# Performance work log

Measured on AMD Instinct MI355X. Metric: run time of the kernel, lower is better.

Reference implementation:

```python
import jax, jax.numpy as jnp
import numpy as np

C = 512
NH = 8
HD = C // NH
GROUPS = 8
EPS = 1e-5

def group_norm(x, w, b):
    # x: [B,C,H,W], 8 groups
    B, Cc, H, W = x.shape
    xg = x.reshape(B, GROUPS, Cc // GROUPS, H, W)
    mu = xg.mean(axis=(2, 3, 4), keepdims=True)
    var = xg.var(axis=(2, 3, 4), keepdims=True)
    xn = (xg - mu) * jax.lax.rsqrt(var + EPS)
    xn = xn.reshape(B, Cc, H, W)
    return xn * w[None, :, None, None] + b[None, :, None, None]

def conv1x1(x, w, b):
    # w: [O,C], b: [O]
    return jnp.einsum('oc,bchw->bohw', w, x) + b[None, :, None, None]

def setup_inputs() -> dict:
    key = jax.random.key(0)
    ks = jax.random.split(key, 12)
    s = 1.0 / np.sqrt(C)
    inp = {
        'x': jax.random.normal(ks[0], (8, C, 32, 32), dtype=jnp.float32),
        'norm_w': jnp.ones((C,), jnp.float32),
        'norm_b': jnp.zeros((C,), jnp.float32),
        'qw': jax.random.uniform(ks[1], (C, C), jnp.float32, -s, s),
        'qb': jax.random.uniform(ks[2], (C,), jnp.float32, -s, s),
        'kw': jax.random.uniform(ks[3], (C, C), jnp.float32, -s, s),
        'kb': jax.random.uniform(ks[4], (C,), jnp.float32, -s, s),
        'vw': jax.random.uniform(ks[5], (C, C), jnp.float32, -s, s),
        'vb': jax.random.uniform(ks[6], (C,), jnp.float32, -s, s),
        'pw': jax.random.uniform(ks[7], (C, C), jnp.float32, -s, s),
        'pb': jax.random.uniform(ks[8], (C,), jnp.float32, -s, s),
    }
    return inp

def reference(x, norm_w, norm_b, qw, qb, kw, kb, vw, vb, pw, pb):
    b, c, h, w = x.shape
    scale = HD ** (-0.5)
    xn = group_norm(x, norm_w, norm_b)
    q = conv1x1(xn, qw, qb).reshape(b, NH, HD, h * w)
    k = conv1x1(xn, kw, kb).reshape(b, NH, HD, h * w)
    v = conv1x1(xn, vw, vb).reshape(b, NH, HD, h * w)
    attn = jnp.einsum('bhcn,bhcm->bhnm', q, k) * scale
    attn = jax.nn.softmax(attn, axis=-1)
    out = jnp.einsum('bhnm,bhcm->bhcn', attn, v)
    out = out.reshape(b, c, h, w)
    out = conv1x1(out, pw, pb)
    return out + x
```

## Files before the change

kernel.cpp:

```cpp
#include <hip/hip_runtime.h>

#define C_DIM 512
#define N_PIX 1024
#define B_DIM 8
#define NHEAD 8
#define HDIM 64
#define NGRP 8
#define CG 64
#define EPSF 1e-5f

typedef __bf16 bf16x8_t __attribute__((ext_vector_type(8)));
typedef __bf16 bf16x4_t __attribute__((ext_vector_type(4)));
typedef float  f32x4_t  __attribute__((ext_vector_type(4)));
typedef unsigned int u32x4_t __attribute__((ext_vector_type(4)));

__device__ __forceinline__ __bf16 f2b(float f) {
  unsigned int u = __builtin_bit_cast(unsigned int, f);
  u += 0x7fffu + ((u >> 16) & 1u);
  unsigned short s = (unsigned short)(u >> 16);
  return __builtin_bit_cast(__bf16, s);
}

__device__ __forceinline__ unsigned int pack_trunc(float a, float b) {
  return (__builtin_bit_cast(unsigned int, a) >> 16) |
         (__builtin_bit_cast(unsigned int, b) & 0xffff0000u);
}

__device__ __forceinline__ void async16(const void* g, void* l) {
  __builtin_amdgcn_global_load_lds((const __attribute__((address_space(1))) void*)g,
                                   (__attribute__((address_space(3))) void*)l, 16, 0, 0);
}

__global__ __launch_bounds__(256) void prep_kernel(
    const float* __restrict__ qw, const float* __restrict__ kw,
    const float* __restrict__ vw, const float* __restrict__ pw,
    __bf16* __restrict__ wb,
    const float* __restrict__ x, float2* __restrict__ psum)
{
  if (blockIdx.x < 1024) {
    int idx = blockIdx.x * 256 + threadIdx.x;
    int mat = idx >> 16;
    int off = (idx & 65535) * 4;
    const float* src = (mat == 0) ? qw : (mat == 1) ? kw : (mat == 2) ? vw : pw;
    float4 v = *(const float4*)(src + off);
    bf16x4_t pk;
    pk[0] = f2b(v.x); pk[1] = f2b(v.y); pk[2] = f2b(v.z); pk[3] = f2b(v.w);
    *(bf16x4_t*)(wb + mat * (512 * 512) + off) = pk;
  } else {
    const int t = blockIdx.x - 1024;
    const int s = t & 7, bg = t >> 3;
    const float* xp = x + ((size_t)bg * CG + s * 8) * N_PIX;
    float sum = 0.f, sum2 = 0.f;
#pragma unroll
    for (int it = 0; it < 8; it++) {
      float4 v = ((const float4*)xp)[it * 256 + threadIdx.x];
      sum  += v.x + v.y + v.z + v.w;
      sum2 += v.x * v.x + v.y * v.y + v.z * v.z + v.w * v.w;
    }
#pragma unroll
    for (int off = 32; off; off >>= 1) {
      sum  += __shfl_xor(sum, off, 64);
      sum2 += __shfl_xor(sum2, off, 64);
    }
    __shared__ float red[8];
    const int lane = threadIdx.x & 63, wv = threadIdx.x >> 6;
    if (lane == 0) { red[wv] = sum; red[4 + wv] = sum2; }
    __syncthreads();
    if (threadIdx.x == 0) {
      float s1 = red[0] + red[1] + red[2] + red[3];
      float s2 = red[4] + red[5] + red[6] + red[7];
      psum[bg * 8 + s] = make_float2(s1, s2);
    }
  }
}

__global__ __launch_bounds__(256) void gn_apply_kernel(
    const float* __restrict__ x, const float2* __restrict__ psum,
    const float* __restrict__ gw, const float* __restrict__ gb,
    __bf16* __restrict__ xnT)
{
  const int n0 = blockIdx.x * 32, b = blockIdx.y, z = blockIdx.z;
  const int tid = threadIdx.x;
  __shared__ float mu_s[8], rs_s[8];
  __shared__ __align__(16) __bf16 tile[32 * 264];

  if (tid < 8) {
    float s1 = 0.f, s2 = 0.f;
#pragma unroll
    for (int i = 0; i < 8; i++) {
      float2 p = psum[(b * 8 + tid) * 8 + i];
      s1 += p.x; s2 += p.y;
    }
    const float inv = 1.f / (float)(CG * N_PIX);
    float mu = s1 * inv;
    float var = s2 * inv - mu * mu;
    mu_s[tid] = mu;
    rs_s[tid] = rsqrtf(var + EPSF);
  }
  __syncthreads();

  const float* xb = x + (size_t)b * C_DIM * N_PIX + n0;
  const int cl = tid >> 3;
  const int nq = (tid & 7) * 4;
#pragma unroll
  for (int co = 0; co < 8; co++) {
    const int cc = co * 32 + cl;
    const int c = z * 256 + cc;
    float4 v = *(const float4*)(xb + (size_t)c * N_PIX + nq);
    const int g = c >> 6;
    const float rs = rs_s[g];
    const float a = rs * gw[c];
    const float bb = gb[c] - mu_s[g] * a;
    tile[(nq + 0) * 264 + cc] = f2b(v.x * a + bb);
    tile[(nq + 1) * 264 + cc] = f2b(v.y * a + bb);
    tile[(nq + 2) * 264 + cc] = f2b(v.z * a + bb);
    tile[(nq + 3) * 264 + cc] = f2b(v.w * a + bb);
  }
  __syncthreads();

  __bf16* dst = xnT + ((size_t)b * N_PIX + n0) * C_DIM + z * 256;
  const int l32 = tid & 31, nr = tid >> 5;
#pragma unroll
  for (int no = 0; no < 4; no++) {
    const int n = no * 8 + nr;
    const int cc = l32 * 8;
    *(bf16x8_t*)(dst + (size_t)n * C_DIM + cc) =
        *(const bf16x8_t*)(tile + n * 264 + cc);
  }
}

__device__ __forceinline__ void gemm_core_64(
    const __bf16* __restrict__ A, const __bf16* __restrict__ B,
    __bf16* As, __bf16* Bs, f32x4_t acc[2][4])
{
  const int tid  = threadIdx.x;
  const int lane = tid & 63;
  const int wv   = tid >> 6;
  const int quad = lane >> 4;
  const int l16  = lane & 15;
  const int wm = (wv >> 1) * 32;
  const int wn = (wv & 1) * 64;
  const int swq = (quad ^ ((l16 >> 1) & 3)) * 8;

  f32x4_t zero = {0.f, 0.f, 0.f, 0.f};
#pragma unroll
  for (int i = 0; i < 2; i++)
#pragma unroll
    for (int j = 0; j < 4; j++) acc[i][j] = zero;

  const int chA  = wv * 64 + lane;
  const int rA = chA >> 2;
  const int kA = ((chA & 3) ^ ((rA >> 1) & 3)) * 8;
  const int chB0 = wv * 64 + lane, chB1 = 256 + wv * 64 + lane;
  const int rB0 = chB0 >> 2, kB0 = ((chB0 & 3) ^ ((rB0 >> 1) & 3)) * 8;
  const int rB1 = chB1 >> 2, kB1 = ((chB1 & 3) ^ ((rB1 >> 1) & 3)) * 8;

  async16(A + (size_t)rA * 512 + kA,  As + (wv * 64) * 8);
  async16(B + (size_t)rB0 * 512 + kB0, Bs + (wv * 64) * 8);
  async16(B + (size_t)rB1 * 512 + kB1, Bs + (256 + wv * 64) * 8);

  for (int kt2 = 0; kt2 < 8; kt2++) {
#pragma unroll
    for (int pp = 0; pp < 2; pp++) {
      const int pi = kt2 * 2 + pp;
      if (pi < 15) {
        const int kc = (pi + 1) * 32;
        const int nb = (pi + 1) & 1;
        async16(A + (size_t)rA * 512 + kc + kA,  As + nb * 2048 + (wv * 64) * 8);
        async16(B + (size_t)rB0 * 512 + kc + kB0, Bs + nb * 4096 + (wv * 64) * 8);
        async16(B + (size_t)rB1 * 512 + kc + kB1, Bs + nb * 4096 + (256 + wv * 64) * 8);
        asm volatile("s_waitcnt vmcnt(3)" ::: "memory");
      } else {
        asm volatile("s_waitcnt vmcnt(0)" ::: "memory");
      }
      __builtin_amdgcn_s_barrier();
      __builtin_amdgcn_sched_barrier(0);
      bf16x8_t af[2], bfr[4];
#pragma unroll
      for (int i = 0; i < 2; i++)
        af[i] = *(const bf16x8_t*)(As + pp * 2048 + (wm + i * 16 + l16) * 32 + swq);
#pragma unroll
      for (int j = 0; j < 4; j++)
        bfr[j] = *(const bf16x8_t*)(Bs + pp * 4096 + (wn + j * 16 + l16) * 32 + swq);
      __builtin_amdgcn_s_setprio(1);
#pragma unroll
      for (int i = 0; i < 2; i++)
#pragma unroll
        for (int j = 0; j < 4; j++)
          acc[i][j] = __builtin_amdgcn_mfma_f32_16x16x32_bf16(af[i], bfr[j], acc[i][j], 0, 0, 0);
      __builtin_amdgcn_s_setprio(0);
      __builtin_amdgcn_sched_barrier(0);
      __builtin_amdgcn_s_barrier();
    }
  }
}

__global__ __launch_bounds__(256, 2) void gemm_qkv_kernel(
    const __bf16* __restrict__ wqkv, const float* __restrict__ qb,
    const float* __restrict__ kb, const float* __restrict__ vb,
    const __bf16* __restrict__ xnT,
    __bf16* __restrict__ qT, __bf16* __restrict__ kT, __bf16* __restrict__ vbuf)
{
  __shared__ __align__(16) __bf16 smem[20480];
  __bf16* Bs = smem + 12288;
  const int b = blockIdx.x;
  const int n0 = blockIdx.y * 128;
  const int m0 = blockIdx.z * 64;
  const __bf16* Aq = wqkv + (size_t)m0 * 512;
  const __bf16* Ak = Aq + 512 * 512;
  const __bf16* Av = Ak + 512 * 512;
  const __bf16* Bx = xnT + ((size_t)b * N_PIX + n0) * 512;

  const int tid = threadIdx.x, lane = tid & 63, wv = tid >> 6;
  const int quad = lane >> 4, l16 = lane & 15;
  const int wm = (wv >> 1) * 32, wn = (wv & 1) * 64;
  const int swq = (quad ^ ((l16 >> 1) & 3)) * 8;

  const f32x4_t zero = {0.f, 0.f, 0.f, 0.f};
  f32x4_t acc[3][2][4];
#pragma unroll
  for (int m = 0; m < 3; m++)
#pragma unroll
    for (int i = 0; i < 2; i++)
#pragma unroll
      for (int j = 0; j < 4; j++) acc[m][i][j] = zero;

  const int chA = wv * 64 + lane;
  const int rA = chA >> 2;
  const int kA = ((chA & 3) ^ ((rA >> 1) & 3)) * 8;
  const int chB0 = wv * 64 + lane, chB1 = 256 + wv * 64 + lane;
  const int rB0 = chB0 >> 2, kB0 = ((chB0 & 3) ^ ((rB0 >> 1) & 3)) * 8;
  const int rB1 = chB1 >> 2, kB1 = ((chB1 & 3) ^ ((rB1 >> 1) & 3)) * 8;

  async16(Aq + (size_t)rA * 512 + kA, smem + (wv * 64) * 8);
  async16(Ak + (size_t)rA * 512 + kA, smem + 4096 + (wv * 64) * 8);
  async16(Av + (size_t)rA * 512 + kA, smem + 8192 + (wv * 64) * 8);
  async16(Bx + (size_t)rB0 * 512 + kB0, Bs + (wv * 64) * 8);
  async16(Bx + (size_t)rB1 * 512 + kB1, Bs + (256 + wv * 64) * 8);

  for (int kt2 = 0; kt2 < 8; kt2++) {
#pragma unroll
    for (int pp = 0; pp < 2; pp++) {
      const int pi = kt2 * 2 + pp;
      if (pi < 15) {
        const int kc = (pi + 1) * 32;
        const int nb = (pi + 1) & 1;
        async16(Aq + (size_t)rA * 512 + kc + kA, smem + nb * 2048 + (wv * 64) * 8);
        async16(Ak + (size_t)rA * 512 + kc + kA, smem + 4096 + nb * 2048 + (wv * 64) * 8);
        async16(Av + (size_t)rA * 512 + kc + kA, smem + 8192 + nb * 2048 + (wv * 64) * 8);
        async16(Bx + (size_t)rB0 * 512 + kc + kB0, Bs + nb * 4096 + (wv * 64) * 8);
        async16(Bx + (size_t)rB1 * 512 + kc + kB1, Bs + nb * 4096 + (256 + wv * 64) * 8);
        asm volatile("s_waitcnt vmcnt(5)" ::: "memory");
      } else {
        asm volatile("s_waitcnt vmcnt(0)" ::: "memory");
      }
      __builtin_amdgcn_s_barrier();
      __builtin_amdgcn_sched_barrier(0);
      bf16x8_t bfr[4];
#pragma unroll
      for (int j = 0; j < 4; j++)
        bfr[j] = *(const bf16x8_t*)(Bs + pp * 4096 + (wn + j * 16 + l16) * 32 + swq);
#pragma unroll
      for (int m = 0; m < 3; m++) {
        bf16x8_t af[2];
#pragma unroll
        for (int i = 0; i < 2; i++)
          af[i] = *(const bf16x8_t*)(smem + m * 4096 + pp * 2048 + (wm + i * 16 + l16) * 32 + swq);
        __builtin_amdgcn_s_setprio(1);
#pragma unroll
        for (int i = 0; i < 2; i++)
#pragma unroll
          for (int j = 0; j < 4; j++)
            acc[m][i][j] = __builtin_amdgcn_mfma_f32_16x16x32_bf16(af[i], bfr[j], acc[m][i][j], 0, 0, 0);
        __builtin_amdgcn_s_setprio(0);
      }
      __builtin_amdgcn_sched_barrier(0);
      __builtin_amdgcn_s_barrier();
    }
  }

  const float qscale = 0.125f * 1.44269504f;
#pragma unroll
  for (int mat = 0; mat < 2; mat++) {
    const float* bias = (mat == 0) ? qb : kb;
    const float sc = (mat == 0) ? qscale : 1.0f;
    __bf16* dst = (mat == 0) ? qT : kT;
#pragma unroll
    for (int i = 0; i < 2; i++) {
      const int crow = wm + i * 16 + quad * 4;
      const int o = m0 + crow;
      float b0 = bias[o], b1 = bias[o + 1], b2 = bias[o + 2], b3 = bias[o + 3];
#pragma unroll
      for (int j = 0; j < 4; j++) {
        const int nl = wn + j * 16 + l16;
        bf16x4_t pk;
        pk[0] = f2b((acc[mat][i][j][0] + b0) * sc);
        pk[1] = f2b((acc[mat][i][j][1] + b1) * sc);
        pk[2] = f2b((acc[mat][i][j][2] + b2) * sc);
        pk[3] = f2b((acc[mat][i][j][3] + b3) * sc);
        *(bf16x4_t*)(smem + nl * 72 + crow) = pk;
      }
    }
    __syncthreads();
#pragma unroll
    for (int it = 0; it < 4; it++) {
      const int n = it * 32 + (tid >> 3);
      const int c = (tid & 7) * 8;
      *(bf16x8_t*)(dst + ((size_t)b * N_PIX + n0 + n) * 512 + m0 + c) =
          *(const bf16x8_t*)(smem + n * 72 + c);
    }
    __syncthreads();
  }
#pragma unroll
  for (int i = 0; i < 2; i++) {
    const int crow = wm + i * 16 + quad * 4;
    const int o = m0 + crow;
    float b0 = vb[o], b1 = vb[o + 1], b2 = vb[o + 2], b3 = vb[o + 3];
#pragma unroll
    for (int j = 0; j < 4; j++) {
      const int nl = wn + j * 16 + l16;
      smem[(crow + 0) * 132 + nl] = f2b(acc[2][i][j][0] + b0);
      smem[(crow + 1) * 132 + nl] = f2b(acc[2][i][j][1] + b1);
      smem[(crow + 2) * 132 + nl] = f2b(acc[2][i][j][2] + b2);
      smem[(crow + 3) * 132 + nl] = f2b(acc[2][i][j][3] + b3);
    }
  }
  __syncthreads();
  {
    const int c = tid >> 2;
    const int nch = (tid & 3) * 32;
    __bf16* vd = vbuf + ((size_t)b * 512 + m0 + c) * N_PIX + n0 + nch;
#pragma unroll
    for (int k = 0; k < 4; k++)
      *(bf16x8_t*)(vd + k * 8) = *(const bf16x8_t*)(smem + c * 132 + nch + k * 8);
  }
}

__global__ __launch_bounds__(256, 2) void attn_kernel(
    const __bf16* __restrict__ qT, const __bf16* __restrict__ kT,
    const __bf16* __restrict__ vbuf, __bf16* __restrict__ aT)
{
  __shared__ __align__(16) __bf16 Ks[2][64 * 72];
  __shared__ __align__(16) __bf16 Vp[2][64 * 72];
  const int bh = blockIdx.x;
  const int b = bh >> 3, head = bh & 7;
  const int n0 = blockIdx.y * 128;
  const int tid = threadIdx.x, lane = tid & 63, wv = tid >> 6;
  const int quad = lane >> 4, l16 = lane & 15;

  bf16x8_t qf[2][2];
#pragma unroll
  for (int qt = 0; qt < 2; qt++) {
    const __bf16* qp = qT + ((size_t)b * N_PIX + n0 + wv * 32 + qt * 16 + l16) * 512 + head * 64;
    qf[qt][0] = *(const bf16x8_t*)(qp + quad * 8);
    qf[qt][1] = *(const bf16x8_t*)(qp + 32 + quad * 8);
  }

  const __bf16* kp = kT + ((size_t)b * N_PIX) * 512 + head * 64;
  const __bf16* vp = vbuf + ((size_t)b * 512 + head * 64) * N_PIX;

  const int srow = tid >> 2, scol = (tid & 3) * 16;
  const int pr0 = scol >> 5, hh0 = (scol >> 4) & 1;
  const int pos0 = pr0 * 32 + ((scol >> 2) & 3) * 8 + hh0 * 4;
  const int mc1 = scol + 8;
  const int pr1 = mc1 >> 5, hh1 = (mc1 >> 4) & 1;
  const int pos1 = pr1 * 32 + ((mc1 >> 2) & 3) * 8 + hh1 * 4;

  bf16x8_t kreg0 = *(const bf16x8_t*)(kp + (size_t)srow * 512 + scol);
  bf16x8_t kreg1 = *(const bf16x8_t*)(kp + (size_t)srow * 512 + scol + 8);
  bf16x8_t vreg0 = *(const bf16x8_t*)(vp + (size_t)srow * N_PIX + scol);
  bf16x8_t vreg1 = *(const bf16x8_t*)(vp + (size_t)srow * N_PIX + scol + 8);
  {
    *(bf16x8_t*)(Ks[0] + srow * 72 + scol)     = kreg0;
    *(bf16x8_t*)(Ks[0] + srow * 72 + scol + 8) = kreg1;
    bf16x4_t lo, hi;
#pragma unroll
    for (int r = 0; r < 4; r++) { lo[r] = vreg0[r]; hi[r] = vreg0[4 + r]; }
    *(bf16x4_t*)(Vp[0] + srow * 72 + pos0)     = lo;
    *(bf16x4_t*)(Vp[0] + srow * 72 + pos0 + 8) = hi;
#pragma unroll
    for (int r = 0; r < 4; r++) { lo[r] = vreg1[r]; hi[r] = vreg1[4 + r]; }
    *(bf16x4_t*)(Vp[0] + srow * 72 + pos1)     = lo;
    *(bf16x4_t*)(Vp[0] + srow * 72 + pos1 + 8) = hi;
  }
  kreg0 = *(const bf16x8_t*)(kp + (size_t)(64 + srow) * 512 + scol);
  kreg1 = *(const bf16x8_t*)(kp + (size_t)(64 + srow) * 512 + scol + 8);
  vreg0 = *(const bf16x8_t*)(vp + (size_t)srow * N_PIX + 64 + scol);
  vreg1 = *(const bf16x8_t*)(vp + (size_t)srow * N_PIX + 64 + scol + 8);
  asm volatile("s_waitcnt lgkmcnt(0)" ::: "memory");
  __builtin_amdgcn_s_barrier();
  __builtin_amdgcn_sched_barrier(0);

  const f32x4_t zero = {0.f, 0.f, 0.f, 0.f};
  f32x4_t oacc[2][4];
#pragma unroll
  for (int qt = 0; qt < 2; qt++)
#pragma unroll
    for (int jc = 0; jc < 4; jc++) oacc[qt][jc] = zero;
  f32x4_t lsum4[2] = {zero, zero};

  for (int mt = 0; mt < 16; mt++) {
    const int cur = mt & 1, nxt = cur ^ 1;
    const __bf16* Kc = Ks[cur];
    const __bf16* Vc = Vp[cur];

    f32x4_t sacc[2][4];
    __builtin_amdgcn_s_setprio(1);
#pragma unroll
    for (int mb = 0; mb < 4; mb++) {
      bf16x8_t kf0 = *(const bf16x8_t*)(Kc + (mb * 16 + l16) * 72 + quad * 8);
      bf16x8_t kf1 = *(const bf16x8_t*)(Kc + (mb * 16 + l16) * 72 + 32 + quad * 8);
#pragma unroll
      for (int qt = 0; qt < 2; qt++) {
        f32x4_t s = zero;
        s = __builtin_amdgcn_mfma_f32_16x16x32_bf16(kf0, qf[qt][0], s, 0, 0, 0);
        s = __builtin_amdgcn_mfma_f32_16x16x32_bf16(kf1, qf[qt][1], s, 0, 0, 0);
        sacc[qt][mb] = s;
      }
    }
    __builtin_amdgcn_s_setprio(0);

    bf16x8_t pf[2][2];
#pragma unroll
    for (int qt = 0; qt < 2; qt++) {
      float p[4][4];
#pragma unroll
      for (int mb = 0; mb < 4; mb++)
#pragma unroll
        for (int r = 0; r < 4; r++) {
          p[mb][r] = __builtin_amdgcn_exp2f(sacc[qt][mb][r]);
          lsum4[qt][r] += p[mb][r];
        }
#pragma unroll
      for (int pr = 0; pr < 2; pr++) {
        u32x4_t u;
        u[0] = pack_trunc(p[2 * pr][0],     p[2 * pr][1]);
        u[1] = pack_trunc(p[2 * pr][2],     p[2 * pr][3]);
        u[2] = pack_trunc(p[2 * pr + 1][0], p[2 * pr + 1][1]);
        u[3] = pack_trunc(p[2 * pr + 1][2], p[2 * pr + 1][3]);
        pf[qt][pr] = __builtin_bit_cast(bf16x8_t, u);
      }
    }

    __builtin_amdgcn_s_setprio(1);
#pragma unroll
    for (int jc = 0; jc < 4; jc++) {
      const int vrow = (jc * 16 + l16) * 72;
#pragma unroll
      for (int pr = 0; pr < 2; pr++) {
        bf16x8_t vf = *(const bf16x8_t*)(Vc + vrow + pr * 32 + quad * 8);
#pragma unroll
        for (int qt = 0; qt < 2; qt++)
          oacc[qt][jc] = __builtin_amdgcn_mfma_f32_16x16x32_bf16(vf, pf[qt][pr], oacc[qt][jc], 0, 0, 0);
      }
    }
    __builtin_amdgcn_s_setprio(0);

    if (mt < 15) {
      *(bf16x8_t*)(Ks[nxt] + srow * 72 + scol)     = kreg0;
      *(bf16x8_t*)(Ks[nxt] + srow * 72 + scol + 8) = kreg1;
      bf16x4_t lo, hi;
#pragma unroll
      for (int r = 0; r < 4; r++) { lo[r] = vreg0[r]; hi[r] = vreg0[4 + r]; }
      *(bf16x4_t*)(Vp[nxt] + srow * 72 + pos0)     = lo;
      *(bf16x4_t*)(Vp[nxt] + srow * 72 + pos0 + 8) = hi;
#pragma unroll
      for (int r = 0; r < 4; r++) { lo[r] = vreg1[r]; hi[r] = vreg1[4 + r]; }
      *(bf16x4_t*)(Vp[nxt] + srow * 72 + pos1)     = lo;
      *(bf16x4_t*)(Vp[nxt] + srow * 72 + pos1 + 8) = hi;
      if (mt < 14) {
        kreg0 = *(const bf16x8_t*)(kp + (size_t)((mt + 2) * 64 + srow) * 512 + scol);
        kreg1 = *(const bf16x8_t*)(kp + (size_t)((mt + 2) * 64 + srow) * 512 + scol + 8);
        vreg0 = *(const bf16x8_t*)(vp + (size_t)srow * N_PIX + (mt + 2) * 64 + scol);
        vreg1 = *(const bf16x8_t*)(vp + (size_t)srow * N_PIX + (mt + 2) * 64 + scol + 8);
      }
      asm volatile("s_waitcnt lgkmcnt(0)" ::: "memory");
      __builtin_amdgcn_s_barrier();
      __builtin_amdgcn_sched_barrier(0);
    }
  }

  __syncthreads();
  __bf16* Tr = &Ks[0][0];
#pragma unroll
  for (int qt = 0; qt < 2; qt++) {
    float lsum = lsum4[qt][0] + lsum4[qt][1] + lsum4[qt][2] + lsum4[qt][3];
    lsum += __shfl_xor(lsum, 16, 64);
    lsum += __shfl_xor(lsum, 32, 64);
    const float inv = 1.f / lsum;
    const int nl = wv * 32 + qt * 16 + l16;
#pragma unroll
    for (int jc = 0; jc < 4; jc++) {
      bf16x4_t o4;
#pragma unroll
      for (int r = 0; r < 4; r++) o4[r] = f2b(oacc[qt][jc][r] * inv);
      *(bf16x4_t*)(Tr + nl * 72 + jc * 16 + quad * 4) = o4;
    }
  }
  __syncthreads();
#pragma unroll
  for (int it = 0; it < 4; it++) {
    const int n = it * 32 + (tid >> 3);
    const int c = (tid & 7) * 8;
    *(bf16x8_t*)(aT + ((size_t)b * N_PIX + n0 + n) * 512 + head * 64 + c) =
        *(const bf16x8_t*)(Tr + n * 72 + c);
  }
}

__global__ __launch_bounds__(256, 4) void gemm_proj_kernel(
    const __bf16* __restrict__ wp, const float* __restrict__ pb,
    const __bf16* __restrict__ aT, const float* __restrict__ x,
    float* __restrict__ out)
{
  __shared__ __align__(16) __bf16 smem[12288];
  __bf16* As = smem;
  __bf16* Bs = smem + 4096;
  const int b = blockIdx.x;
  const int n0 = blockIdx.y * 128;
  const int m0 = blockIdx.z * 64;
  const __bf16* A = wp + (size_t)m0 * 512;
  const __bf16* B = aT + ((size_t)b * N_PIX + n0) * 512;
  f32x4_t acc[2][4];
  gemm_core_64(A, B, As, Bs, acc);
  const int tid = threadIdx.x, lane = tid & 63, wv = tid >> 6;
  const int quad = lane >> 4, l16 = lane & 15;
  const int wm = (wv >> 1) * 32, wn = (wv & 1) * 64;
#pragma unroll
  for (int i = 0; i < 2; i++) {
    const int o = m0 + wm + i * 16 + quad * 4;
#pragma unroll
    for (int j = 0; j < 4; j++) {
      const int n = n0 + wn + j * 16 + l16;
#pragma unroll
      for (int r = 0; r < 4; r++) {
        size_t idx = ((size_t)b * 512 + o + r) * N_PIX + n;
        out[idx] = acc[i][j][r] + pb[o + r] + x[idx];
      }
    }
  }
}

extern "C" void kernel_launch(void* const* d_in, const int* in_sizes, int n_in,
                              void* d_out, int out_size, void* d_ws, size_t ws_size,
                              hipStream_t stream)
{
  (void)in_sizes; (void)n_in; (void)out_size; (void)ws_size;
  const float* x   = (const float*)d_in[0];
  const float* gnw = (const float*)d_in[1];
  const float* gnb = (const float*)d_in[2];
  const float* qw  = (const float*)d_in[3];
  const float* qb  = (const float*)d_in[4];
  const float* kw  = (const float*)d_in[5];
  const float* kb  = (const float*)d_in[6];
  const float* vw  = (const float*)d_in[7];
  const float* vb  = (const float*)d_in[8];
  const float* pw  = (const float*)d_in[9];
  const float* pb  = (const float*)d_in[10];
  float* out = (float*)d_out;

  char* ws = (char*)d_ws;
  __bf16* wb   = (__bf16*)(ws);
  __bf16* xnT  = (__bf16*)(ws + (size_t)(2  << 20));
  __bf16* qTb  = (__bf16*)(ws + (size_t)(10 << 20));
  __bf16* kTb  = (__bf16*)(ws + (size_t)(18 << 20));
  __bf16* vbf  = (__bf16*)(ws + (size_t)(26 << 20));
  __bf16* aT   = (__bf16*)(ws + (size_t)(34 << 20));
  float2* psum = (float2*)(ws + (size_t)(42 << 20));

  hipLaunchKernelGGL(prep_kernel, dim3(1536), dim3(256), 0, stream,
                     qw, kw, vw, pw, wb, x, psum);
  hipLaunchKernelGGL(gn_apply_kernel, dim3(32, 8, 2), dim3(256), 0, stream, x, psum, gnw, gnb, xnT);
  hipLaunchKernelGGL(gemm_qkv_kernel, dim3(8, 8, 8), dim3(256), 0, stream,
                     wb, qb, kb, vb, xnT, qTb, kTb, vbf);
  hipLaunchKernelGGL(attn_kernel, dim3(64, 8), dim3(256), 0, stream, qTb, kTb, vbf, aT);
  hipLaunchKernelGGL(gemm_proj_kernel, dim3(8, 8, 8), dim3(256), 0, stream,
                     wb + (size_t)3 * 512 * 512, pb, aT, x, out);
}
```

Before: 148.3 us.

## Switch QKV and projection GEMM main loops to three-stage async pipelines

The QKV and projection GEMM kernels move from double-buffered to triple-buffered shared-memory staging. Two k-tiles are prefetched ahead, with vmcnt waits adjusted so each step waits only for the oldest tile. The loop is fully unrolled and uses a p%3 buffer index. This aims to hide more global-load latency behind MFMA work, at the cost of more LDS per block (60KB for QKV, 36KB for proj), which may limit occupancy.

```diff
diff --git a/kernel.cpp b/kernel.cpp
--- a/kernel.cpp
+++ b/kernel.cpp
@@ -131,7 +131,7 @@
 
 __device__ __forceinline__ void gemm_core_64(
     const __bf16* __restrict__ A, const __bf16* __restrict__ B,
-    __bf16* As, __bf16* Bs, f32x4_t acc[2][4])
+    __bf16* smem, f32x4_t acc[2][4])
 {
   const int tid  = threadIdx.x;
   const int lane = tid & 63;
@@ -155,43 +155,45 @@
   const int rB0 = chB0 >> 2, kB0 = ((chB0 & 3) ^ ((rB0 >> 1) & 3)) * 8;
   const int rB1 = chB1 >> 2, kB1 = ((chB1 & 3) ^ ((rB1 >> 1) & 3)) * 8;
 
-  async16(A + (size_t)rA * 512 + kA,  As + (wv * 64) * 8);
-  async16(B + (size_t)rB0 * 512 + kB0, Bs + (wv * 64) * 8);
-  async16(B + (size_t)rB1 * 512 + kB1, Bs + (256 + wv * 64) * 8);
-
-  for (int kt2 = 0; kt2 < 8; kt2++) {
-#pragma unroll
-    for (int pp = 0; pp < 2; pp++) {
-      const int pi = kt2 * 2 + pp;
-      if (pi < 15) {
-        const int kc = (pi + 1) * 32;
-        const int nb = (pi + 1) & 1;
-        async16(A + (size_t)rA * 512 + kc + kA,  As + nb * 2048 + (wv * 64) * 8);
-        async16(B + (size_t)rB0 * 512 + kc + kB0, Bs + nb * 4096 + (wv * 64) * 8);
-        async16(B + (size_t)rB1 * 512 + kc + kB1, Bs + nb * 4096 + (256 + wv * 64) * 8);
-        asm volatile("s_waitcnt vmcnt(3)" ::: "memory");
-      } else {
-        asm volatile("s_waitcnt vmcnt(0)" ::: "memory");
-      }
-      __builtin_amdgcn_s_barrier();
-      __builtin_amdgcn_sched_barrier(0);
-      bf16x8_t af[2], bfr[4];
-#pragma unroll
-      for (int i = 0; i < 2; i++)
-        af[i] = *(const bf16x8_t*)(As + pp * 2048 + (wm + i * 16 + l16) * 32 + swq);
+  auto STAGE = [&](int p) {
+    const int kc = p * 32;
+    __bf16* base = smem + (p % 3) * 6144;
+    async16(A + (size_t)rA * 512 + kc + kA,  base + (wv * 64) * 8);
+    async16(B + (size_t)rB0 * 512 + kc + kB0, base + 2048 + (wv * 64) * 8);
+    async16(B + (size_t)rB1 * 512 + kc + kB1, base + 2048 + (256 + wv * 64) * 8);
+  };
+
+  STAGE(0); STAGE(1);
+
+#pragma unroll
+  for (int p = 0; p < 16; p++) {
+    if (p <= 13) {
+      STAGE(p + 2);
+      asm volatile("s_waitcnt vmcnt(6)" ::: "memory");
+    } else if (p == 14) {
+      asm volatile("s_waitcnt vmcnt(3)" ::: "memory");
+    } else {
+      asm volatile("s_waitcnt vmcnt(0)" ::: "memory");
+    }
+    __builtin_amdgcn_s_barrier();
+    __builtin_amdgcn_sched_barrier(0);
+    const __bf16* base = smem + (p % 3) * 6144;
+    bf16x8_t af[2], bfr[4];
+#pragma unroll
+    for (int i = 0; i < 2; i++)
+      af[i] = *(const bf16x8_t*)(base + (wm + i * 16 + l16) * 32 + swq);
+#pragma unroll
+    for (int j = 0; j < 4; j++)
+      bfr[j] = *(const bf16x8_t*)(base + 2048 + (wn + j * 16 + l16) * 32 + swq);
+    __builtin_amdgcn_s_setprio(1);
+#pragma unroll
+    for (int i = 0; i < 2; i++)
 #pragma unroll
       for (int j = 0; j < 4; j++)
-        bfr[j] = *(const bf16x8_t*)(Bs + pp * 4096 + (wn + j * 16 + l16) * 32 + swq);
-      __builtin_amdgcn_s_setprio(1);
-#pragma unroll
-      for (int i = 0; i < 2; i++)
-#pragma unroll
-        for (int j = 0; j < 4; j++)
-          acc[i][j] = __builtin_amdgcn_mfma_f32_16x16x32_bf16(af[i], bfr[j], acc[i][j], 0, 0, 0);
-      __builtin_amdgcn_s_setprio(0);
-      __builtin_amdgcn_sched_barrier(0);
-      __builtin_amdgcn_s_barrier();
-    }
+        acc[i][j] = __builtin_amdgcn_mfma_f32_16x16x32_bf16(af[i], bfr[j], acc[i][j], 0, 0, 0);
+    __builtin_amdgcn_s_setprio(0);
+    __builtin_amdgcn_sched_barrier(0);
+    __builtin_amdgcn_s_barrier();
   }
 }
 
@@ -201,8 +203,7 @@
     const __bf16* __restrict__ xnT,
     __bf16* __restrict__ qT, __bf16* __restrict__ kT, __bf16* __restrict__ vbuf)
 {
-  __shared__ __align__(16) __bf16 smem[20480];
-  __bf16* Bs = smem + 12288;
+  __shared__ __align__(16) __bf16 smem[30720];
   const int b = blockIdx.x;
   const int n0 = blockIdx.y * 128;
   const int m0 = blockIdx.z * 64;
@@ -232,51 +233,51 @@
   const int rB0 = chB0 >> 2, kB0 = ((chB0 & 3) ^ ((rB0 >> 1) & 3)) * 8;
   const int rB1 = chB1 >> 2, kB1 = ((chB1 & 3) ^ ((rB1 >> 1) & 3)) * 8;
 
-  async16(Aq + (size_t)rA * 512 + kA, smem + (wv * 64) * 8);
-  async16(Ak + (size_t)rA * 512 + kA, smem + 4096 + (wv * 64) * 8);
-  async16(Av + (size_t)rA * 512 + kA, smem + 8192 + (wv * 64) * 8);
-  async16(Bx + (size_t)rB0 * 512 + kB0, Bs + (wv * 64) * 8);
-  async16(Bx + (size_t)rB1 * 512 + kB1, Bs + (256 + wv * 64) * 8);
-
-  for (int kt2 = 0; kt2 < 8; kt2++) {
-#pragma unroll
-    for (int pp = 0; pp < 2; pp++) {
-      const int pi = kt2 * 2 + pp;
-      if (pi < 15) {
-        const int kc = (pi + 1) * 32;
-        const int nb = (pi + 1) & 1;
-        async16(Aq + (size_t)rA * 512 + kc + kA, smem + nb * 2048 + (wv * 64) * 8);
-        async16(Ak + (size_t)rA * 512 + kc + kA, smem + 4096 + nb * 2048 + (wv * 64) * 8);
-        async16(Av + (size_t)rA * 512 + kc + kA, smem + 8192 + nb * 2048 + (wv * 64) * 8);
-        async16(Bx + (size_t)rB0 * 512 + kc + kB0, Bs + nb * 4096 + (wv * 64) * 8);
-        async16(Bx + (size_t)rB1 * 512 + kc + kB1, Bs + nb * 4096 + (256 + wv * 64) * 8);
-        asm volatile("s_waitcnt vmcnt(5)" ::: "memory");
-      } else {
-        asm volatile("s_waitcnt vmcnt(0)" ::: "memory");
-      }
-      __builtin_amdgcn_s_barrier();
-      __builtin_amdgcn_sched_barrier(0);
-      bf16x8_t bfr[4];
-#pragma unroll
-      for (int j = 0; j < 4; j++)
-        bfr[j] = *(const bf16x8_t*)(Bs + pp * 4096 + (wn + j * 16 + l16) * 32 + swq);
-#pragma unroll
-      for (int m = 0; m < 3; m++) {
-        bf16x8_t af[2];
-#pragma unroll
-        for (int i = 0; i < 2; i++)
-          af[i] = *(const bf16x8_t*)(smem + m * 4096 + pp * 2048 + (wm + i * 16 + l16) * 32 + swq);
-        __builtin_amdgcn_s_setprio(1);
-#pragma unroll
-        for (int i = 0; i < 2; i++)
-#pragma unroll
-          for (int j = 0; j < 4; j++)
-            acc[m][i][j] = __builtin_amdgcn_mfma_f32_16x16x32_bf16(af[i], bfr[j], acc[m][i][j], 0, 0, 0);
-        __builtin_amdgcn_s_setprio(0);
-      }
-      __builtin_amdgcn_sched_barrier(0);
-      __builtin_amdgcn_s_barrier();
-    }
+  auto STAGE = [&](int p) {
+    const int kc = p * 32;
+    __bf16* base = smem + (p % 3) * 10240;
+    async16(Aq + (size_t)rA * 512 + kc + kA, base + (wv * 64) * 8);
+    async16(Ak + (size_t)rA * 512 + kc + kA, base + 2048 + (wv * 64) * 8);
+    async16(Av + (size_t)rA * 512 + kc + kA, base + 4096 + (wv * 64) * 8);
+    async16(Bx + (size_t)rB0 * 512 + kc + kB0, base + 6144 + (wv * 64) * 8);
+    async16(Bx + (size_t)rB1 * 512 + kc + kB1, base + 6144 + (256 + wv * 64) * 8);
+  };
+
+  STAGE(0); STAGE(1);
+
+#pragma unroll
+  for (int p = 0; p < 16; p++) {
+    if (p <= 13) {
+      STAGE(p + 2);
+      asm volatile("s_waitcnt vmcnt(10)" ::: "memory");
+    } else if (p == 14) {
+      asm volatile("s_waitcnt vmcnt(5)" ::: "memory");
+    } else {
+      asm volatile("s_waitcnt vmcnt(0)" ::: "memory");
+    }
+    __builtin_amdgcn_s_barrier();
+    __builtin_amdgcn_sched_barrier(0);
+    const __bf16* base = smem + (p % 3) * 10240;
+    bf16x8_t bfr[4];
+#pragma unroll
+    for (int j = 0; j < 4; j++)
+      bfr[j] = *(const bf16x8_t*)(base + 6144 + (wn + j * 16 + l16) * 32 + swq);
+#pragma unroll
+    for (int m = 0; m < 3; m++) {
+      bf16x8_t af[2];
+#pragma unroll
+      for (int i = 0; i < 2; i++)
+        af[i] = *(const bf16x8_t*)(base + m * 2048 + (wm + i * 16 + l16) * 32 + swq);
+      __builtin_amdgcn_s_setprio(1);
+#pragma unroll
+      for (int i = 0; i < 2; i++)
+#pragma unroll
+        for (int j = 0; j < 4; j++)
+          acc[m][i][j] = __builtin_amdgcn_mfma_f32_16x16x32_bf16(af[i], bfr[j], acc[m][i][j], 0, 0, 0);
+      __builtin_amdgcn_s_setprio(0);
+    }
+    __builtin_amdgcn_sched_barrier(0);
+    __builtin_amdgcn_s_barrier();
   }
 
   const float qscale = 0.125f * 1.44269504f;
@@ -512,16 +513,14 @@
     const __bf16* __restrict__ aT, const float* __restrict__ x,
     float* __restrict__ out)
 {
-  __shared__ __align__(16) __bf16 smem[12288];
-  __bf16* As = smem;
-  __bf16* Bs = smem + 4096;
+  __shared__ __align__(16) __bf16 smem[18432];
   const int b = blockIdx.x;
   const int n0 = blockIdx.y * 128;
   const int m0 = blockIdx.z * 64;
   const __bf16* A = wp + (size_t)m0 * 512;
   const __bf16* B = aT + ((size_t)b * N_PIX + n0) * 512;
   f32x4_t acc[2][4];
-  gemm_core_64(A, B, As, Bs, acc);
+  gemm_core_64(A, B, smem, acc);
   const int tid = threadIdx.x, lane = tid & 63, wv = tid >> 6;
   const int quad = lane >> 4, l16 = lane & 15;
   const int wm = (wv >> 1) * 32, wn = (wv & 1) * 64;
```

After: 148.8 us, median of 2. Within noise of the previous version (+0.3%).
